# Kernel optimization log

Hardware: AMD Instinct MI355X
Metric: run time of the kernel (lower is better)

The kernel has to match this reference:

```python
import jax, jax.numpy as jnp
import numpy as np

V, E, H = 50257, 256, 128          # vocab, embedding_size, lstm hidden per direction
L, B = 2048, 64                    # seq_len, batch (x is [L, B], seq-first)
SEP, MASK = 50256, 0
SEP_EVERY = 16
N_UTT = L // SEP_EVERY             # utterances per sequence (seps planted regularly)


def setup_inputs() -> dict:
    key = jax.random.key(0)
    ks = jax.random.split(key, 12)
    x = jax.random.randint(ks[0], (L, B), 0, SEP, dtype=jnp.int32)
    # plant sep tokens every SEP_EVERY positions -> each utterance has SEP_EVERY tokens
    x = x.at[SEP_EVERY - 1::SEP_EVERY, :].set(SEP)
    s = 1.0 / np.sqrt(H)
    u = lambda k, sh: jax.random.uniform(k, sh, jnp.float32, -s, s)
    return {
        "x": x,
        "emb": jax.random.normal(ks[1], (V, E), jnp.float32),
        "w_ih_f": u(ks[2], (4 * H, E)), "w_hh_f": u(ks[3], (4 * H, H)),
        "b_ih_f": u(ks[4], (4 * H,)),   "b_hh_f": u(ks[5], (4 * H,)),
        "w_ih_b": u(ks[6], (4 * H, E)), "w_hh_b": u(ks[7], (4 * H, H)),
        "b_ih_b": u(ks[8], (4 * H,)),   "b_hh_b": u(ks[9], (4 * H,)),
        "w_out": u(ks[10], (2, E)),     "b_out": u(ks[11], (2,)),
    }


def _lstm_dir(xu, w_ih, w_hh, b_ih, b_hh, reverse):
    # xu: [T, B, E]; PyTorch LSTM gate order i, f, g, o
    xp = jnp.einsum("tbe,ge->tbg", xu, w_ih) + b_ih + b_hh  # [T, B, 4H]

    def step(carry, xt):
        h, c = carry
        g = xt + h @ w_hh.T
        i, f, gg, o = jnp.split(g, 4, axis=-1)
        c = jax.nn.sigmoid(f) * c + jax.nn.sigmoid(i) * jnp.tanh(gg)
        h = jax.nn.sigmoid(o) * jnp.tanh(c)
        return (h, c), h

    init = (jnp.zeros((xu.shape[1], H), xu.dtype), jnp.zeros((xu.shape[1], H), xu.dtype))
    _, hs = jax.lax.scan(step, init, xp, reverse=reverse)
    return hs  # [T, B, H]


def _forward(x, emb, w_ih_f, w_hh_f, b_ih_f, b_hh_f, w_ih_b, w_hh_b, b_ih_b, b_hh_b, w_out, b_out):
    # --- ragged utterance mean-pool (replaces per-token Python loops) ---
    seps = (x == SEP)
    seg = jnp.cumsum(seps.astype(jnp.int32), axis=0) - seps.astype(jnp.int32)  # [L,B]: utterance id per token (sep ends its utterance)
    gids = (seg * B + jnp.arange(B, dtype=jnp.int32)[None, :]).reshape(L * B)
    tok_emb = emb[x]                                              # [L, B, E]
    sums = jax.ops.segment_sum(tok_emb.reshape(L * B, E), gids, num_segments=N_UTT * B).reshape(N_UTT, B, E)
    cnts = jax.ops.segment_sum(jnp.ones((L * B,), tok_emb.dtype), gids, num_segments=N_UTT * B).reshape(N_UTT, B, 1)
    u = jnp.where(cnts > 0, sums / jnp.maximum(cnts, 1.0), 0.0)   # [N_UTT, B, E] (zeros pad, as original)
    # --- BiLSTM over utterances ---
    h_f = _lstm_dir(u, w_ih_f, w_hh_f, b_ih_f, b_hh_f, reverse=False)
    h_b = _lstm_dir(u, w_ih_b, w_hh_b, b_ih_b, b_hh_b, reverse=True)
    h = jnp.concatenate([h_f, h_b], axis=-1)                      # [N_UTT, B, E]
    logits = jnp.einsum("tbe,oe->tbo", h, w_out) + b_out          # [N_UTT, B, 2]
    policy = jax.nn.softmax(logits, axis=-1)
    # greedy policy (deterministic reference)
    u_mask = jnp.argmax(policy, axis=-1)                          # [N_UTT, B] in {0,1}
    chosen_policy = jnp.take_along_axis(policy, u_mask[..., None], axis=-1)  # [N_UTT, B, 1]
    # expand utterance mask to token mask and mask the input
    token_mask = u_mask.astype(bool)[seg, jnp.arange(B)[None, :]]  # [L, B]
    masked_input = jnp.where(token_mask, x, MASK)
    return logits, policy, chosen_policy, u_mask.astype(bool), masked_input


def reference(x, emb, w_ih_f, w_hh_f, b_ih_f, b_hh_f, w_ih_b, w_hh_b, b_ih_b, b_hh_b, w_out, b_out):
    return _forward(x, emb, w_ih_f, w_hh_f, b_ih_f, b_hh_f, w_ih_b, w_hh_b, b_ih_b, b_hh_b, w_out, b_out)
```

## Files before the change

kernel.cpp:

```cpp
#include <hip/hip_runtime.h>
#include <math.h>

#define LL   2048
#define BB   64
#define EE   256
#define HH   128
#define GG   512
#define TT   128
#define SEPT 50256

__global__ __launch_bounds__(256) void segscan_k(
    const int* __restrict__ x, int* __restrict__ seg,
    int* __restrict__ cnt, int* __restrict__ start)
{
    int b   = blockIdx.x;
    int tid = threadIdx.x;
    __shared__ int tsum[256];
    __shared__ int ucnt[TT];
    __shared__ int ustart[TT];

    int flags[8];
    int local = 0;
#pragma unroll
    for (int i = 0; i < 8; i++) {
        int t = tid * 8 + i;
        flags[i] = (x[t * BB + b] == SEPT) ? 1 : 0;
        local += flags[i];
    }
    tsum[tid] = local;
    __syncthreads();
    int val = local;
    for (int off = 1; off < 256; off <<= 1) {
        int other = (tid >= off) ? tsum[tid - off] : 0;
        __syncthreads();
        val += other;
        tsum[tid] = val;
        __syncthreads();
    }
    int excl = val - local;

    if (tid < TT) ucnt[tid] = 0;
    __syncthreads();
    int run = excl;
#pragma unroll
    for (int i = 0; i < 8; i++) {
        int t = tid * 8 + i;
        int s = run;
        seg[t * BB + b] = s;
        run += flags[i];
        if (s < TT) atomicAdd(&ucnt[s], 1);
    }
    __syncthreads();
    if (tid == 0) {
        int acc = 0;
        for (int u = 0; u < TT; u++) { ustart[u] = acc; acc += ucnt[u]; }
    }
    __syncthreads();
    if (tid < TT) {
        cnt[tid * BB + b]   = ucnt[tid];
        start[tid * BB + b] = ustart[tid];
    }
}

__global__ __launch_bounds__(256) void pool_k(
    const int* __restrict__ x, const float* __restrict__ emb,
    const int* __restrict__ cnt, const int* __restrict__ start,
    float* __restrict__ up)
{
    int wid  = threadIdx.x >> 6;
    int lane = threadIdx.x & 63;
    int bid  = blockIdx.x * 4 + wid;
    int b    = bid & 63;
    int c    = cnt[bid];
    int st   = start[bid];

    float4 acc = {0.f, 0.f, 0.f, 0.f};
    int tok = (c > 0) ? x[st * BB + b] : 0;
    for (int j = 0; j < c; j++) {
        int tok_n = (j + 1 < c) ? x[(st + j + 1) * BB + b] : 0;
        float4 v = ((const float4*)(emb + (size_t)tok * EE))[lane];
        acc.x += v.x; acc.y += v.y; acc.z += v.z; acc.w += v.w;
        tok = tok_n;
    }
    float inv = (c > 0) ? 1.f / (float)c : 0.f;
    float4 r = {acc.x * inv, acc.y * inv, acc.z * inv, acc.w * inv};
    ((float4*)(up + (size_t)bid * EE))[lane] = r;
}

__global__ __launch_bounds__(256) void xp_gemm_k(
    const float* __restrict__ A,
    const float* __restrict__ wf, const float* __restrict__ wb,
    const float* __restrict__ bihf, const float* __restrict__ bhhf,
    const float* __restrict__ bihb, const float* __restrict__ bhhb,
    float* __restrict__ C)
{
    __shared__ float As[32][128];
    __shared__ float Bs[32][128];
    int tid  = threadIdx.x;
    int row0 = blockIdx.x * 128;
    int col0 = blockIdx.y * 128;
    int tx = tid & 15, ty = tid >> 4;
    float acc[8][8] = {};

    for (int k0 = 0; k0 < EE; k0 += 32) {
#pragma unroll
        for (int i = 0; i < 4; i++) {
            int idx = tid + i * 256;
            int m   = idx >> 3;
            int k4  = idx & 7;
            float4 av = *(const float4*)(A + (size_t)(row0 + m) * EE + k0 + k4 * 4);
            As[k4 * 4 + 0][m] = av.x; As[k4 * 4 + 1][m] = av.y;
            As[k4 * 4 + 2][m] = av.z; As[k4 * 4 + 3][m] = av.w;
        }
#pragma unroll
        for (int i = 0; i < 4; i++) {
            int idx = tid + i * 256;
            int n   = idx >> 3;
            int k4  = idx & 7;
            int gc  = col0 + n;
            const float* wsrc = (gc < GG) ? (wf + (size_t)gc * EE)
                                          : (wb + (size_t)(gc - GG) * EE);
            float4 bv = *(const float4*)(wsrc + k0 + k4 * 4);
            Bs[k4 * 4 + 0][n] = bv.x; Bs[k4 * 4 + 1][n] = bv.y;
            Bs[k4 * 4 + 2][n] = bv.z; Bs[k4 * 4 + 3][n] = bv.w;
        }
        __syncthreads();
#pragma unroll
        for (int k = 0; k < 32; k++) {
            float a8[8], b8[8];
            *(float4*)&a8[0] = *(const float4*)&As[k][ty * 8 + 0];
            *(float4*)&a8[4] = *(const float4*)&As[k][ty * 8 + 4];
            *(float4*)&b8[0] = *(const float4*)&Bs[k][tx * 8 + 0];
            *(float4*)&b8[4] = *(const float4*)&Bs[k][tx * 8 + 4];
#pragma unroll
            for (int i = 0; i < 8; i++)
#pragma unroll
                for (int j = 0; j < 8; j++)
                    acc[i][j] += a8[i] * b8[j];
        }
        __syncthreads();
    }

    float bias[8];
#pragma unroll
    for (int j = 0; j < 8; j++) {
        int gc = col0 + tx * 8 + j;
        bias[j] = (gc < GG) ? (bihf[gc] + bhhf[gc])
                            : (bihb[gc - GG] + bhhb[gc - GG]);
    }
#pragma unroll
    for (int i = 0; i < 8; i++) {
        int r = row0 + ty * 8 + i;
        float4 v0 = {acc[i][0] + bias[0], acc[i][1] + bias[1],
                     acc[i][2] + bias[2], acc[i][3] + bias[3]};
        float4 v1 = {acc[i][4] + bias[4], acc[i][5] + bias[5],
                     acc[i][6] + bias[6], acc[i][7] + bias[7]};
        *(float4*)(C + (size_t)r * 1024 + col0 + tx * 8 + 0) = v0;
        *(float4*)(C + (size_t)r * 1024 + col0 + tx * 8 + 4) = v1;
    }
}

__device__ __forceinline__ float sigm_f(float x) {
    return 1.f / (1.f + __expf(-x));
}
__device__ __forceinline__ float tanh_f(float x) {
    return 1.f - 2.f / (__expf(2.f * x) + 1.f);
}

__global__ __launch_bounds__(512, 2) void lstm_rec_k(
    const float* __restrict__ xp,
    const float* __restrict__ whh_f, const float* __restrict__ whh_b,
    float* __restrict__ hout)
{
    int bid = blockIdx.x;
    int dir = bid >> 6;
    int b   = bid & 63;
    int tid = threadIdx.x;
    int wv  = tid >> 6;
    int l   = tid & 63;
    const float* whh = dir ? whh_b : whh_f;

    float w[8][16];
#pragma unroll
    for (int j = 0; j < 8; j++) {
        const float* src = whh + (size_t)(l + 64 * j) * HH + 16 * wv;
#pragma unroll
        for (int k4 = 0; k4 < 4; k4++) {
            float4 wv4 = *(const float4*)(src + k4 * 4);
            w[j][k4 * 4 + 0] = wv4.x; w[j][k4 * 4 + 1] = wv4.y;
            w[j][k4 * 4 + 2] = wv4.z; w[j][k4 * 4 + 3] = wv4.w;
        }
    }

    __shared__ __align__(16) float h_lds[HH];
    __shared__ float part[GG][9];
    __shared__ float act[GG];

    int g    = tid;
    int sect = g >> 7;

    float c = 0.f;
    if (g < HH) h_lds[g] = 0.f;
    __syncthreads();

    int t0   = dir ? (TT - 1) : 0;
    float xg = xp[(size_t)(t0 * BB + b) * 1024 + dir * GG + g];

    for (int s = 0; s < TT; s++) {
        float hs[16];
#pragma unroll
        for (int k4 = 0; k4 < 4; k4++)
            *(float4*)&hs[k4 * 4] = *(const float4*)&h_lds[wv * 16 + k4 * 4];

        float acc[8] = {0.f, 0.f, 0.f, 0.f, 0.f, 0.f, 0.f, 0.f};
#pragma unroll
        for (int k = 0; k < 16; k++) {
            float hk = hs[k];
#pragma unroll
            for (int j = 0; j < 8; j++)
                acc[j] += w[j][k] * hk;
        }

        float xg_next = xg;
        if (s < TT - 1) {
            int tn = dir ? (TT - 2 - s) : (s + 1);
            xg_next = xp[(size_t)(tn * BB + b) * 1024 + dir * GG + g];
        }

#pragma unroll
        for (int j = 0; j < 8; j++)
            part[l + 64 * j][wv] = acc[j];
        __syncthreads();

        float sum = xg;
#pragma unroll
        for (int w2 = 0; w2 < 8; w2++)
            sum += part[g][w2];
        act[g] = (sect == 2) ? tanh_f(sum) : sigm_f(sum);
        __syncthreads();

        if (tid < HH) {
            float si = act[tid], sf = act[HH + tid];
            float tg = act[2 * HH + tid], so = act[3 * HH + tid];
            c = sf * c + si * tg;
            float h = so * tanh_f(c);
            h_lds[tid] = h;
            int t = dir ? (TT - 1 - s) : s;
            hout[((size_t)(dir * TT + t) * BB + b) * HH + tid] = h;
        }
        xg = xg_next;
        __syncthreads();
    }
}

__global__ __launch_bounds__(256) void head_k(
    const float* __restrict__ hbuf,
    const float* __restrict__ wout, const float* __restrict__ bout,
    float* __restrict__ out)
{
    int wid  = threadIdx.x >> 6;
    int lane = threadIdx.x & 63;
    int row  = blockIdx.x * 4 + wid;
    int t = row >> 6, b = row & 63;
    const float* hf = hbuf + ((size_t)(t)      * BB + b) * HH;
    const float* hb = hbuf + ((size_t)(TT + t) * BB + b) * HH;

    float l0 = 0.f, l1 = 0.f, v;
    v = hf[lane];      l0 += v * wout[lane];           l1 += v * wout[256 + lane];
    v = hf[lane + 64]; l0 += v * wout[64 + lane];      l1 += v * wout[320 + lane];
    v = hb[lane];      l0 += v * wout[128 + lane];     l1 += v * wout[384 + lane];
    v = hb[lane + 64]; l0 += v * wout[192 + lane];     l1 += v * wout[448 + lane];
#pragma unroll
    for (int off = 32; off > 0; off >>= 1) {
        l0 += __shfl_down(l0, off);
        l1 += __shfl_down(l1, off);
    }
    if (lane == 0) {
        l0 += bout[0]; l1 += bout[1];
        float m  = fmaxf(l0, l1);
        float e0 = __expf(l0 - m), e1 = __expf(l1 - m);
        float inv = 1.f / (e0 + e1);
        float p0 = e0 * inv, p1 = e1 * inv;
        int amax = (l1 > l0) ? 1 : 0;
        out[(size_t)row * 2 + 0] = l0;
        out[(size_t)row * 2 + 1] = l1;
        out[16384 + (size_t)row * 2 + 0] = p0;
        out[16384 + (size_t)row * 2 + 1] = p1;
        out[32768 + row] = amax ? p1 : p0;
        out[40960 + row] = (float)amax;
    }
}

__global__ __launch_bounds__(256) void mask_k(
    const int* __restrict__ x, const int* __restrict__ seg,
    const float* __restrict__ umask, float* __restrict__ out4)
{
    int idx = blockIdx.x * 256 + threadIdx.x;
    int b = idx & 63;
    int s = seg[idx];
    if (s > TT - 1) s = TT - 1;
    if (s < 0) s = 0;
    float keep = umask[s * BB + b];
    out4[idx] = (keep != 0.f) ? (float)x[idx] : 0.f;
}

extern "C" void kernel_launch(void* const* d_in, const int* in_sizes, int n_in,
                              void* d_out, int out_size, void* d_ws, size_t ws_size,
                              hipStream_t stream)
{
    const int*   x    = (const int*)  d_in[0];
    const float* emb  = (const float*)d_in[1];
    const float* wihf = (const float*)d_in[2];
    const float* whhf = (const float*)d_in[3];
    const float* bihf = (const float*)d_in[4];
    const float* bhhf = (const float*)d_in[5];
    const float* wihb = (const float*)d_in[6];
    const float* whhb = (const float*)d_in[7];
    const float* bihb = (const float*)d_in[8];
    const float* bhhb = (const float*)d_in[9];
    const float* wout = (const float*)d_in[10];
    const float* bout = (const float*)d_in[11];
    float* out = (float*)d_out;
    char*  ws  = (char*)d_ws;

    int*   seg   = (int*)  (ws + 0);
    int*   cnt   = (int*)  (ws + 524288);
    int*   start = (int*)  (ws + 557056);
    float* up    = (float*)(ws + 589824);
    float* xp    = (float*)(ws + 8978432);
    float* hbuf  = (float*)(ws + 42532864);

    segscan_k<<<64, 256, 0, stream>>>(x, seg, cnt, start);
    pool_k<<<2048, 256, 0, stream>>>(x, emb, cnt, start, up);
    xp_gemm_k<<<dim3(64, 8), 256, 0, stream>>>(up, wihf, wihb, bihf, bhhf, bihb, bhhb, xp);
    lstm_rec_k<<<128, 512, 0, stream>>>(xp, whhf, whhb, hbuf);
    head_k<<<2048, 256, 0, stream>>>(hbuf, wout, bout, out);
    mask_k<<<512, 256, 0, stream>>>(x, seg, out + 40960, out + 49152);
}
```

Before: 298.7 us.

## Stream fp16 recurrent weights from cache instead of holding fp32 in registers

A new conversion kernel turns both W_hh matrices into fp16 in a thread-contiguous layout, writing into the pooled-utterance buffer once the input GEMM no longer needs it. The recurrent LSTM kernel no longer keeps 128 fp32 weights per thread in registers. Each step it reloads its 8x16 fp16 slice with vector loads and converts it to fp32 before the FMAs. This frees registers to help occupancy or avoid spills, but adds per-step global/L1 loads, conversion work, an extra launch, and fp16 rounding of the weights.

```diff
diff --git a/kernel.cpp b/kernel.cpp
--- a/kernel.cpp
+++ b/kernel.cpp
@@ -1,4 +1,5 @@
 #include <hip/hip_runtime.h>
+#include <hip/hip_fp16.h>
 #include <math.h>
 
 #define LL   2048
@@ -167,9 +168,23 @@
     return 1.f - 2.f / (__expf(2.f * x) + 1.f);
 }
 
+__global__ __launch_bounds__(256) void cvt_k(
+    const float* __restrict__ wf, const float* __restrict__ wb,
+    __half* __restrict__ o)
+{
+    int i = blockIdx.x * 256 + threadIdx.x;
+    int k   = i & 15;
+    int l   = (i >> 4) & 63;
+    int j   = (i >> 10) & 7;
+    int wv  = (i >> 13) & 7;
+    int dir = i >> 16;
+    const float* src = dir ? wb : wf;
+    o[i] = __float2half(src[(l + 64 * j) * HH + 16 * wv + k]);
+}
+
 __global__ __launch_bounds__(512, 2) void lstm_rec_k(
     const float* __restrict__ xp,
-    const float* __restrict__ whh_f, const float* __restrict__ whh_b,
+    const __half* __restrict__ wh16,
     float* __restrict__ hout)
 {
     int bid = blockIdx.x;
@@ -178,19 +193,8 @@
     int tid = threadIdx.x;
     int wv  = tid >> 6;
     int l   = tid & 63;
-    const float* whh = dir ? whh_b : whh_f;
-
-    float w[8][16];
-#pragma unroll
-    for (int j = 0; j < 8; j++) {
-        const float* src = whh + (size_t)(l + 64 * j) * HH + 16 * wv;
-#pragma unroll
-        for (int k4 = 0; k4 < 4; k4++) {
-            float4 wv4 = *(const float4*)(src + k4 * 4);
-            w[j][k4 * 4 + 0] = wv4.x; w[j][k4 * 4 + 1] = wv4.y;
-            w[j][k4 * 4 + 2] = wv4.z; w[j][k4 * 4 + 3] = wv4.w;
-        }
-    }
+    const __half* wh = wh16 + (size_t)dir * (GG * HH);
+    const __half* wbase = wh + (((size_t)wv * 8) * 64 + l) * 16;
 
     __shared__ __align__(16) float h_lds[HH];
     __shared__ float part[GG][9];
@@ -214,11 +218,21 @@
 
         float acc[8] = {0.f, 0.f, 0.f, 0.f, 0.f, 0.f, 0.f, 0.f};
 #pragma unroll
-        for (int k = 0; k < 16; k++) {
-            float hk = hs[k];
-#pragma unroll
-            for (int j = 0; j < 8; j++)
-                acc[j] += w[j][k] * hk;
+        for (int j = 0; j < 8; j++) {
+            float4 q0 = *(const float4*)(wbase + (size_t)j * 1024);
+            float4 q1 = *(const float4*)(wbase + (size_t)j * 1024 + 8);
+            const __half2* ha = (const __half2*)&q0;
+            const __half2* hb = (const __half2*)&q1;
+#pragma unroll
+            for (int p = 0; p < 4; p++) {
+                acc[j] = fmaf(__low2float(ha[p]),  hs[2 * p + 0], acc[j]);
+                acc[j] = fmaf(__high2float(ha[p]), hs[2 * p + 1], acc[j]);
+            }
+#pragma unroll
+            for (int p = 0; p < 4; p++) {
+                acc[j] = fmaf(__low2float(hb[p]),  hs[8 + 2 * p + 0], acc[j]);
+                acc[j] = fmaf(__high2float(hb[p]), hs[8 + 2 * p + 1], acc[j]);
+            }
         }
 
         float xg_next = xg;
@@ -329,11 +343,13 @@
     float* up    = (float*)(ws + 589824);
     float* xp    = (float*)(ws + 8978432);
     float* hbuf  = (float*)(ws + 42532864);
+    __half* wh16 = (__half*)up;
 
     segscan_k<<<64, 256, 0, stream>>>(x, seg, cnt, start);
     pool_k<<<2048, 256, 0, stream>>>(x, emb, cnt, start, up);
     xp_gemm_k<<<dim3(64, 8), 256, 0, stream>>>(up, wihf, wihb, bihf, bhhf, bihb, bhhb, xp);
-    lstm_rec_k<<<128, 512, 0, stream>>>(xp, whhf, whhb, hbuf);
+    cvt_k<<<512, 256, 0, stream>>>(whhf, whhb, wh16);
+    lstm_rec_k<<<128, 512, 0, stream>>>(xp, wh16, hbuf);
     head_k<<<2048, 256, 0, stream>>>(hbuf, wout, bout, out);
     mask_k<<<512, 256, 0, stream>>>(x, seg, out + 40960, out + 49152);
 }
```

Measured after the change: 294.8 us. No clear change (-1.3%).
